# Kernel optimization log

Measured on AMD Instinct MI355X. Metric: run time of the kernel, lower is better.

The kernel has to match this reference:

```python
import math
import jax, jax.numpy as jnp
import numpy as np

B, S, D, H = 2, 2048, 2048, 16  # batch, seq, d_model, n_heads


def setup_inputs() -> dict:
    key = jax.random.key(0)
    ks = jax.random.split(key, 5)
    w_scale = 1.0 / math.sqrt(D)
    return {
        "x": jax.random.normal(ks[0], (B, S, D), jnp.float32),
        "attn_bias": jax.random.normal(ks[1], (1, H, S, S), jnp.float32) * 0.1,
        "Wqkv_w": jax.random.normal(ks[2], (3 * D, D), jnp.float32) * w_scale,
        "Wqkv_b": jnp.zeros((3 * D,), jnp.float32),
        "out_w": jax.random.normal(ks[3], (D, D), jnp.float32) * w_scale,
        "out_b": jnp.zeros((D,), jnp.float32),
    }


def reference(x, attn_bias, Wqkv_w, Wqkv_b, out_w, out_b):
    b, s, d = x.shape
    hd = d // H                      # head dim = 128
    scale = 1.0 / math.sqrt(hd)      # module default: 1/sqrt(d_model // n_heads)

    # fused QKV projection
    qkv = x @ Wqkv_w.T + Wqkv_b                       # [b, s, 3d]
    q, k, v = jnp.split(qkv, 3, axis=2)               # each [b, s, d]
    q = q.reshape(b, s, H, hd).transpose(0, 2, 1, 3)  # [b, h, s, hd]
    k = k.reshape(b, s, H, hd).transpose(0, 2, 1, 3)
    v = v.reshape(b, s, H, hd).transpose(0, 2, 1, 3)

    # scaled scores + additive bias (bias sliced to trailing q/k lengths)
    scores = jnp.einsum('bhqd,bhkd->bhqk', q, k) * scale
    scores = scores + attn_bias[:, :, -s:, -s:]

    # causal mask, masked positions set to dtype min (matches masked_fill with finfo.min)
    causal = jnp.tril(jnp.ones((s, s), dtype=bool))   # True = keep
    min_val = jnp.finfo(scores.dtype).min
    scores = jnp.where(causal[None, None, :, :], scores, min_val)

    p = jax.nn.softmax(scores, axis=-1)               # [b, h, s, s]
    out = jnp.einsum('bhqk,bhkd->bhqd', p, v)         # [b, h, s, hd]
    out = out.transpose(0, 2, 1, 3).reshape(b, s, d)  # [b, s, d]

    return out @ out_w.T + out_b
```

## Files before the change

### kernel.cpp

```cpp
#include <hip/hip_runtime.h>
#include <hip/hip_bf16.h>
#include <stdint.h>

#define H_  16
#define S_  2048
#define D_  2048
#define HD_ 128

typedef __bf16 bf16x8 __attribute__((ext_vector_type(8)));
typedef short  s16x8  __attribute__((ext_vector_type(8)));
typedef float  f32x4  __attribute__((ext_vector_type(4)));
typedef unsigned short u16x4 __attribute__((ext_vector_type(4)));

__device__ __forceinline__ unsigned short f2bf(float f) {
    unsigned u = __builtin_bit_cast(unsigned, f);
    u += 0x7fffu + ((u >> 16) & 1u);
    return (unsigned short)(u >> 16);
}

__device__ __forceinline__ bf16x8 ld_bf8(const unsigned short* p) {
    s16x8 r = *reinterpret_cast<const s16x8*>(p);
    return __builtin_bit_cast(bf16x8, r);
}

#define GLOAD_LDS16(gp, lp)                                                     \
    __builtin_amdgcn_global_load_lds(                                            \
        (const __attribute__((address_space(1))) void*)(gp),                     \
        (__attribute__((address_space(3))) void*)(lp), 16, 0, 0)

__global__ __launch_bounds__(256) void cast3_f32_bf16(const float* __restrict__ i0,
                                                      unsigned short* __restrict__ o0,
                                                      const float* __restrict__ i1,
                                                      unsigned short* __restrict__ o1,
                                                      const float* __restrict__ i2,
                                                      unsigned short* __restrict__ o2) {
    const int bid = blockIdx.x;
    const float* in;
    unsigned short* out;
    int base;
    if (bid < 8192)       { in = i0; out = o0; base = bid; }
    else if (bid < 20480) { in = i1; out = o1; base = bid - 8192; }
    else                  { in = i2; out = o2; base = bid - 20480; }
    int i = (base * 256 + threadIdx.x) * 4;
    float4 v = *reinterpret_cast<const float4*>(in + i);
    u16x4 o;
    o[0] = f2bf(v.x); o[1] = f2bf(v.y); o[2] = f2bf(v.z); o[3] = f2bf(v.w);
    *reinterpret_cast<u16x4*>(out + i) = o;
}

__device__ __forceinline__ void gemm128_core(const unsigned short* __restrict__ Aptr,
                                             const unsigned short* __restrict__ Bptr,
                                             int m0, int n0,
                                             unsigned short* As, unsigned short* Bs,
                                             f32x4 acc[4][4]) {
    const int t  = threadIdx.x;
    const int l  = t & 63, w = t >> 6;
    const int wr = w >> 1, wc = w & 1;
    const int lr = l & 15, g = l >> 4;

    f32x4 zero = {0.f, 0.f, 0.f, 0.f};
#pragma unroll
    for (int i = 0; i < 4; ++i)
#pragma unroll
        for (int j = 0; j < 4; ++j) acc[i][j] = zero;

    for (int kt = 0; kt < D_; kt += 64) {
#pragma unroll
        for (int p = 0; p < 4; ++p) {
            int lin = (p * 256 + t) * 16;
            int row = lin >> 7, colb = lin & 127;
            int scol = (colb ^ ((row & 7) << 4)) >> 1;
            GLOAD_LDS16(Aptr + (size_t)(m0 + row) * D_ + kt + scol, &As[lin >> 1]);
        }
#pragma unroll
        for (int p = 0; p < 4; ++p) {
            int lin = (p * 256 + t) * 16;
            int row = lin >> 7, colb = lin & 127;
            int scol = (colb ^ ((row & 7) << 4)) >> 1;
            GLOAD_LDS16(Bptr + (size_t)(n0 + row) * D_ + kt + scol, &Bs[lin >> 1]);
        }
        __syncthreads();
#pragma unroll
        for (int ks = 0; ks < 2; ++ks) {
            bf16x8 af[4], bfr[4];
#pragma unroll
            for (int mi = 0; mi < 4; ++mi)
                af[mi] = ld_bf8(&As[(wr * 64 + mi * 16 + lr) * 64 +
                                    ((ks * 32 + g * 8) ^ ((lr & 7) << 3))]);
#pragma unroll
            for (int ni = 0; ni < 4; ++ni)
                bfr[ni] = ld_bf8(&Bs[(wc * 64 + ni * 16 + lr) * 64 +
                                     ((ks * 32 + g * 8) ^ ((lr & 7) << 3))]);
#pragma unroll
            for (int mi = 0; mi < 4; ++mi)
#pragma unroll
                for (int ni = 0; ni < 4; ++ni)
                    acc[mi][ni] = __builtin_amdgcn_mfma_f32_16x16x32_bf16(
                        af[mi], bfr[ni], acc[mi][ni], 0, 0, 0);
        }
        __syncthreads();
    }
}

__global__ __launch_bounds__(256) void gemm_bt_qkv(const unsigned short* __restrict__ A,
                                                   const unsigned short* __restrict__ W,
                                                   const float* __restrict__ bias,
                                                   unsigned short* __restrict__ Qo,
                                                   unsigned short* __restrict__ Ko,
                                                   unsigned short* __restrict__ Vo) {
    __shared__ alignas(16) unsigned short As[128 * 64];
    __shared__ alignas(16) unsigned short Bs[128 * 64];

    const int GX = 48, NWG = 1536, CPX = NWG / 8;
    const int raw = blockIdx.y * GX + blockIdx.x;
    const int swz = (raw & 7) * CPX + (raw >> 3);
    const int m0 = (swz / GX) * 128, n0 = (swz % GX) * 128;

    f32x4 acc[4][4];
    gemm128_core(A, W, m0, n0, As, Bs, acc);

    const int l  = threadIdx.x & 63, w = threadIdx.x >> 6;
    const int wr = w >> 1, wc = w & 1;
    const int lr = l & 15, g = l >> 4;

    const int which = n0 >> 11;
    const int h     = (n0 & 2047) >> 7;
    const int b     = m0 >> 11;
    const int sb    = m0 & 2047;

    float bias_v[4];
#pragma unroll
    for (int ni = 0; ni < 4; ++ni)
        bias_v[ni] = bias[n0 + wc * 64 + ni * 16 + lr];

    if (which == 2) {
        unsigned short* Vb = Vo + ((size_t)(b * H_ + h)) * HD_ * S_;
#pragma unroll
        for (int mi = 0; mi < 4; ++mi) {
#pragma unroll
            for (int ni = 0; ni < 4; ++ni) {
                int d = wc * 64 + ni * 16 + lr;
                int s = sb + wr * 64 + mi * 16 + g * 4;
                u16x4 pv;
#pragma unroll
                for (int i = 0; i < 4; ++i) pv[i] = f2bf(acc[mi][ni][i] + bias_v[ni]);
                *reinterpret_cast<u16x4*>(&Vb[(size_t)d * S_ + s]) = pv;
            }
        }
    } else {
        unsigned short* Pb = ((which == 0) ? Qo : Ko) + ((size_t)(b * H_ + h)) * S_ * HD_;
#pragma unroll
        for (int mi = 0; mi < 4; ++mi) {
#pragma unroll
            for (int ni = 0; ni < 4; ++ni) {
                int d = wc * 64 + ni * 16 + lr;
#pragma unroll
                for (int i = 0; i < 4; ++i) {
                    int s = sb + wr * 64 + mi * 16 + g * 4 + i;
                    Pb[(size_t)s * HD_ + d] = f2bf(acc[mi][ni][i] + bias_v[ni]);
                }
            }
        }
    }
}

__global__ __launch_bounds__(256) void gemm_bt_out(const unsigned short* __restrict__ A,
                                                   const unsigned short* __restrict__ W,
                                                   const float* __restrict__ bias,
                                                   float* __restrict__ out) {
    __shared__ alignas(16) unsigned short As[128 * 64];
    __shared__ alignas(16) unsigned short Bs[128 * 64];

    const int GX = 16, NWG = 512, CPX = NWG / 8;
    const int raw = blockIdx.y * GX + blockIdx.x;
    const int swz = (raw & 7) * CPX + (raw >> 3);
    const int m0 = (swz / GX) * 128, n0 = (swz % GX) * 128;

    f32x4 acc[4][4];
    gemm128_core(A, W, m0, n0, As, Bs, acc);

    const int l  = threadIdx.x & 63, w = threadIdx.x >> 6;
    const int wr = w >> 1, wc = w & 1;
    const int lr = l & 15, g = l >> 4;

    for (int mi = 0; mi < 4; ++mi) {
        for (int ni = 0; ni < 4; ++ni) {
            for (int i = 0; i < 4; ++i) {
                int m = m0 + wr * 64 + mi * 16 + g * 4 + i;
                int n = n0 + wc * 64 + ni * 16 + lr;
                out[(size_t)m * D_ + n] = acc[mi][ni][i] + bias[n];
            }
        }
    }
}

__global__ __launch_bounds__(256) void attn_kernel11(const unsigned short* __restrict__ Q,
                                                     const unsigned short* __restrict__ K,
                                                     const unsigned short* __restrict__ Vt,
                                                     const float* __restrict__ biasPtr,
                                                     unsigned short* __restrict__ O) {
    __shared__ alignas(16) unsigned short Klds[3][4096];
    __shared__ alignas(16) unsigned short Vlds[3][4096];
    __shared__ alignas(16) unsigned short Pbuf[4][16 * 32];

    const int t  = threadIdx.x;
    const int l  = t & 63, w = t >> 6;
    const int lr = l & 15, g = l >> 4;

    const int raw   = blockIdx.x;
    const int xcd   = raw & 7;
    const int local = raw >> 3;
    const int cu    = local & 31;
    const int slot  = local >> 5;
    const int qt    = (slot & 1) ? cu : (31 - cu);
    const int bh    = xcd + 8 * slot;
    const int b     = bh >> 4, head = bh & 15;

    const unsigned short* Qb = Q + (size_t)bh * S_ * HD_;
    const unsigned short* Kb = K + (size_t)bh * S_ * HD_;
    const unsigned short* Vb = Vt + (size_t)bh * HD_ * S_;
    const float* Bh32 = biasPtr + (size_t)head * S_ * S_;
    const float scale = 0.08838834764831845f;

    const int q0 = qt * 64 + w * 16;

    bf16x8 qf[4];
#pragma unroll
    for (int dc = 0; dc < 4; ++dc)
        qf[dc] = ld_bf8(Qb + (size_t)(q0 + lr) * HD_ + dc * 32 + g * 8);

    f32x4 zero = {0.f, 0.f, 0.f, 0.f};
    f32x4 o[8];
#pragma unroll
    for (int nc = 0; nc < 8; ++nc) o[nc] = zero;
    float lp[4] = {0.f, 0.f, 0.f, 0.f};

    unsigned short* Pw = Pbuf[w];

    auto STAGE = [&](int buf, int k0) {
#pragma unroll
        for (int p = 0; p < 2; ++p) {
            int lin = p * 4096 + t * 16;
            int row = lin >> 8;
            int colb = lin & 255;
            int scolb = colb ^ ((row & 7) << 4);
            GLOAD_LDS16(Kb + (size_t)(k0 + row) * HD_ + (scolb >> 1), &Klds[buf][lin >> 1]);
        }
#pragma unroll
        for (int p = 0; p < 2; ++p) {
            int lin = p * 4096 + t * 16;
            int row = lin >> 6;
            int colb = lin & 63;
            int scolb = colb ^ ((row & 3) << 4);
            GLOAD_LDS16(Vb + (size_t)row * S_ + k0 + (scolb >> 1), &Vlds[buf][lin >> 1]);
        }
    };

    const int nch = 2 * qt + 2;

    STAGE(0, 0);
    STAGE(1, 32);
    asm volatile("s_waitcnt vmcnt(4)" ::: "memory");
    __builtin_amdgcn_s_barrier();

    int cur = 0;
    for (int c = 0; c < nch; ++c) {
        const int k0 = c * 32;

        float bias_r[4][2];
#pragma unroll
        for (int i = 0; i < 4; ++i) {
            const int boff = (q0 + g * 4 + i) * S_ + k0 + lr;
#pragma unroll
            for (int kc = 0; kc < 2; ++kc)
                bias_r[i][kc] = Bh32[boff + kc * 16];
        }

        int s2 = cur + 2; if (s2 >= 3) s2 -= 3;
        if (c + 2 < nch) STAGE(s2, k0 + 64);

        f32x4 s[2];
        s[0] = zero; s[1] = zero;
#pragma unroll
        for (int kc = 0; kc < 2; ++kc) {
            bf16x8 kf[4];
#pragma unroll
            for (int dc = 0; dc < 4; ++dc)
                kf[dc] = ld_bf8(&Klds[cur][(kc * 16 + lr) * 128 + ((dc * 32 + g * 8) ^ ((lr & 7) << 3))]);
#pragma unroll
            for (int dc = 0; dc < 4; ++dc)
                s[kc] = __builtin_amdgcn_mfma_f32_16x16x32_bf16(qf[dc], kf[dc], s[kc], 0, 0, 0);
        }

        const bool maskzone = (c >= nch - 2);
#pragma unroll
        for (int i = 0; i < 4; ++i) {
            const int rowabs = q0 + g * 4 + i;
            const int prow   = g * 4 + i;
            float e[2];
#pragma unroll
            for (int kc = 0; kc < 2; ++kc) {
                float v = s[kc][i] * scale + bias_r[i][kc];
                if (maskzone && (k0 + kc * 16 + lr > rowabs)) v = -1.0e30f;
                e[kc] = __expf(v - 16.0f);
            }
            lp[i] += e[0] + e[1];
            const int sw = (prow & 3) << 3;
            Pw[(prow * 32 + 0  + lr) ^ sw] = f2bf(e[0]);
            Pw[(prow * 32 + 16 + lr) ^ sw] = f2bf(e[1]);
        }

        {
            bf16x8 pa = ld_bf8(&Pw[lr * 32 + ((g * 8) ^ ((lr & 3) << 3))]);
#pragma unroll
            for (int nc = 0; nc < 8; ++nc) {
                bf16x8 vf = ld_bf8(&Vlds[cur][(nc * 16 + lr) * 32 + ((g * 8) ^ ((lr & 3) << 3))]);
                o[nc] = __builtin_amdgcn_mfma_f32_16x16x32_bf16(pa, vf, o[nc], 0, 0, 0);
            }
        }

        if (c + 1 < nch) {
            if (c + 2 < nch) { asm volatile("s_waitcnt vmcnt(4)" ::: "memory"); }
            else             { asm volatile("s_waitcnt vmcnt(0)" ::: "memory"); }
            __builtin_amdgcn_s_barrier();
        }
        cur = (cur == 2) ? 0 : cur + 1;
    }

#pragma unroll
    for (int i = 0; i < 4; ++i) {
        lp[i] += __shfl_xor(lp[i], 1);
        lp[i] += __shfl_xor(lp[i], 2);
        lp[i] += __shfl_xor(lp[i], 4);
        lp[i] += __shfl_xor(lp[i], 8);
    }

#pragma unroll
    for (int i = 0; i < 4; ++i) {
        float inv = 1.0f / lp[i];
        int row = q0 + g * 4 + i;
#pragma unroll
        for (int nc = 0; nc < 8; ++nc) {
            O[((size_t)(b * S_ + row)) * D_ + head * HD_ + nc * 16 + lr] = f2bf(o[nc][i] * inv);
        }
    }
}

extern "C" void kernel_launch(void* const* d_in, const int* in_sizes, int n_in,
                              void* d_out, int out_size, void* d_ws, size_t ws_size,
                              hipStream_t stream) {
    (void)in_sizes; (void)n_in; (void)out_size; (void)ws_size;
    const float* x         = (const float*)d_in[0];
    const float* attn_bias = (const float*)d_in[1];
    const float* Wqkv_w    = (const float*)d_in[2];
    const float* Wqkv_b    = (const float*)d_in[3];
    const float* out_w     = (const float*)d_in[4];
    const float* out_b     = (const float*)d_in[5];
    float* out = (float*)d_out;

    char* ws = (char*)d_ws;
    unsigned short* xb    = (unsigned short*)(ws);
    unsigned short* wqkvb = (unsigned short*)(ws + 16777216);
    unsigned short* woutb = (unsigned short*)(ws + 41943040);
    unsigned short* Qb    = (unsigned short*)(ws + 50331648);
    unsigned short* Kb    = (unsigned short*)(ws + 67108864);
    unsigned short* Vtb   = (unsigned short*)(ws + 83886080);
    unsigned short* Ob    = xb;

    cast3_f32_bf16<<<24576, 256, 0, stream>>>(x, xb, Wqkv_w, wqkvb, out_w, woutb);
    gemm_bt_qkv<<<dim3(48, 32), 256, 0, stream>>>(xb, wqkvb, Wqkv_b, Qb, Kb, Vtb);
    attn_kernel11<<<1024, 256, 0, stream>>>(Qb, Kb, Vtb, attn_bias, Ob);
    gemm_bt_out<<<dim3(16, 32), 256, 0, stream>>>(Ob, woutb, out_b, out);
}
```

Measured before the change: 328.4 us.

## Switch attention to double-buffered K/V staging with register-prefetched bias

The attention kernel's LDS staging for K and V drops from three buffers to two, cutting shared memory use, which may allow more resident blocks per CU. The bias for the next chunk is now loaded into registers one iteration ahead instead of at the start of each iteration. The fine-grained vmcnt waits are replaced with a full __syncthreads each iteration, so the prefetch distance shrinks to one chunk and the barrier implicitly drains all outstanding loads, including the bias prefetch. This risks exposing global load latency and adds a few registers for the bias double buffer.

```diff
diff --git a/kernel.cpp b/kernel.cpp
--- a/kernel.cpp
+++ b/kernel.cpp
@@ -194,13 +194,13 @@
     }
 }
 
-__global__ __launch_bounds__(256) void attn_kernel11(const unsigned short* __restrict__ Q,
+__global__ __launch_bounds__(256) void attn_kernel12(const unsigned short* __restrict__ Q,
                                                      const unsigned short* __restrict__ K,
                                                      const unsigned short* __restrict__ Vt,
                                                      const float* __restrict__ biasPtr,
                                                      unsigned short* __restrict__ O) {
-    __shared__ alignas(16) unsigned short Klds[3][4096];
-    __shared__ alignas(16) unsigned short Vlds[3][4096];
+    __shared__ alignas(16) unsigned short Klds[2][4096];
+    __shared__ alignas(16) unsigned short Vlds[2][4096];
     __shared__ alignas(16) unsigned short Pbuf[4][16 * 32];
 
     const int t  = threadIdx.x;
@@ -258,26 +258,33 @@
 
     const int nch = 2 * qt + 2;
 
+    float bias_cur[4][2], bias_nxt[4][2];
+#pragma unroll
+    for (int i = 0; i < 4; ++i) {
+        const int boff = (q0 + g * 4 + i) * S_ + lr;
+        bias_cur[i][0] = Bh32[boff];
+        bias_cur[i][1] = Bh32[boff + 16];
+        bias_nxt[i][0] = 0.f;
+        bias_nxt[i][1] = 0.f;
+    }
+
     STAGE(0, 0);
-    STAGE(1, 32);
-    asm volatile("s_waitcnt vmcnt(4)" ::: "memory");
-    __builtin_amdgcn_s_barrier();
+    __syncthreads();
 
     int cur = 0;
     for (int c = 0; c < nch; ++c) {
         const int k0 = c * 32;
 
-        float bias_r[4][2];
-#pragma unroll
-        for (int i = 0; i < 4; ++i) {
-            const int boff = (q0 + g * 4 + i) * S_ + k0 + lr;
-#pragma unroll
-            for (int kc = 0; kc < 2; ++kc)
-                bias_r[i][kc] = Bh32[boff + kc * 16];
-        }
-
-        int s2 = cur + 2; if (s2 >= 3) s2 -= 3;
-        if (c + 2 < nch) STAGE(s2, k0 + 64);
+        if (c + 1 < nch) {
+#pragma unroll
+            for (int i = 0; i < 4; ++i) {
+                const int boff = (q0 + g * 4 + i) * S_ + (k0 + 32) + lr;
+                bias_nxt[i][0] = Bh32[boff];
+                bias_nxt[i][1] = Bh32[boff + 16];
+            }
+        }
+
+        if (c + 1 < nch) STAGE(cur ^ 1, k0 + 32);
 
         f32x4 s[2];
         s[0] = zero; s[1] = zero;
@@ -300,7 +307,7 @@
             float e[2];
 #pragma unroll
             for (int kc = 0; kc < 2; ++kc) {
-                float v = s[kc][i] * scale + bias_r[i][kc];
+                float v = s[kc][i] * scale + bias_cur[i][kc];
                 if (maskzone && (k0 + kc * 16 + lr > rowabs)) v = -1.0e30f;
                 e[kc] = __expf(v - 16.0f);
             }
@@ -319,12 +326,14 @@
             }
         }
 
-        if (c + 1 < nch) {
-            if (c + 2 < nch) { asm volatile("s_waitcnt vmcnt(4)" ::: "memory"); }
-            else             { asm volatile("s_waitcnt vmcnt(0)" ::: "memory"); }
-            __builtin_amdgcn_s_barrier();
-        }
-        cur = (cur == 2) ? 0 : cur + 1;
+#pragma unroll
+        for (int i = 0; i < 4; ++i) {
+            bias_cur[i][0] = bias_nxt[i][0];
+            bias_cur[i][1] = bias_nxt[i][1];
+        }
+
+        __syncthreads();
+        cur ^= 1;
     }
 
 #pragma unroll
@@ -369,6 +378,6 @@
 
     cast3_f32_bf16<<<24576, 256, 0, stream>>>(x, xb, Wqkv_w, wqkvb, out_w, woutb);
     gemm_bt_qkv<<<dim3(48, 32), 256, 0, stream>>>(xb, wqkvb, Wqkv_b, Qb, Kb, Vtb);
-    attn_kernel11<<<1024, 256, 0, stream>>>(Qb, Kb, Vtb, attn_bias, Ob);
+    attn_kernel12<<<1024, 256, 0, stream>>>(Qb, Kb, Vtb, attn_bias, Ob);
     gemm_bt_out<<<dim3(16, 32), 256, 0, stream>>>(Ob, woutb, out_b, out);
 }
```

After: 328.5 us. Within noise of the previous version (+0.0%).
